# Kernel tuning notes

Measured on AMD Instinct MI355X. Metric: run time of the kernel, lower is better.

## Reference

```python
import jax, jax.numpy as jnp
from jax import lax
import numpy as np

D_MODEL = 512
D_STATE = 16
D_CONV = 4
EXPAND = 2
D_INNER = EXPAND * D_MODEL
DT_RANK = (D_MODEL + 15) // 16  # ceil(d_model/16) = 32
B, L = 4, 1024


def setup_inputs() -> dict:
    key = jax.random.key(0)
    ks = jax.random.split(key, 12)
    s = 0.02
    inp = {
        "feature": jax.random.normal(ks[0], (B, L, D_MODEL), jnp.float32),
        "ln_w": jnp.ones((D_MODEL,), jnp.float32),
        "ln_b": jnp.zeros((D_MODEL,), jnp.float32),
        "in_proj_w": jax.random.normal(ks[1], (2 * D_INNER, D_MODEL), jnp.float32) * s,
        "conv_w": jax.random.normal(ks[2], (D_INNER, D_CONV), jnp.float32) * 0.1,
        "conv_b": jnp.zeros((D_INNER,), jnp.float32),
        "x_proj_w": jax.random.normal(ks[3], (DT_RANK + 2 * D_STATE, D_INNER), jnp.float32) * s,
        "dt_proj_w": jax.random.normal(ks[4], (D_INNER, DT_RANK), jnp.float32) * 0.1,
        "dt_proj_b": jax.random.normal(ks[5], (D_INNER,), jnp.float32) * 0.1 - 4.0,
        "A_log": jnp.log(jnp.broadcast_to(jnp.arange(1, D_STATE + 1, dtype=jnp.float32), (D_INNER, D_STATE))),
        "D": jnp.ones((D_INNER,), jnp.float32),
        "out_proj_w": jax.random.normal(ks[6], (D_MODEL, D_INNER), jnp.float32) * s,
    }
    return inp


def _mamba_block(xn, in_proj_w, conv_w, conv_b, x_proj_w, dt_proj_w, dt_proj_b, A_log, D, out_proj_w):
    # xn: [B, L, d_model]
    xz = jnp.einsum('bld,ed->ble', xn, in_proj_w)          # [B, L, 2*d_inner]
    x, z = xz[..., :D_INNER], xz[..., D_INNER:]
    # causal depthwise conv along L
    xc = jnp.transpose(x, (0, 2, 1))                        # [B, d_inner, L]
    xc = lax.conv_general_dilated(
        xc, conv_w[:, None, :], (1,), [(D_CONV - 1, 0)],
        feature_group_count=D_INNER,
        dimension_numbers=('NCH', 'OIH', 'NCH')) + conv_b[None, :, None]
    x = jax.nn.silu(jnp.transpose(xc, (0, 2, 1)))           # [B, L, d_inner]
    x_dbl = jnp.einsum('bld,ed->ble', x, x_proj_w)          # [B, L, dt_rank+2*d_state]
    dt = x_dbl[..., :DT_RANK]
    Bm = x_dbl[..., DT_RANK:DT_RANK + D_STATE]
    Cm = x_dbl[..., DT_RANK + D_STATE:]
    dt = jax.nn.softplus(jnp.einsum('blr,dr->bld', dt, dt_proj_w) + dt_proj_b)  # [B,L,d_inner]
    A = -jnp.exp(A_log)                                     # [d_inner, d_state]

    def step(h, inp):
        dt_t, B_t, C_t, x_t = inp                           # [B,d_inner],[B,d_state],[B,d_state],[B,d_inner]
        dA = jnp.exp(dt_t[..., None] * A)                   # [B, d_inner, d_state]
        h = dA * h + (dt_t * x_t)[..., None] * B_t[:, None, :]
        y = jnp.einsum('bds,bs->bd', h, C_t)
        return h, y

    xs = (jnp.transpose(dt, (1, 0, 2)), jnp.transpose(Bm, (1, 0, 2)),
          jnp.transpose(Cm, (1, 0, 2)), jnp.transpose(x, (1, 0, 2)))
    h0 = jnp.zeros((xn.shape[0], D_INNER, D_STATE), xn.dtype)
    _, ys = lax.scan(step, h0, xs)                          # ys: [L, B, d_inner]
    y = jnp.transpose(ys, (1, 0, 2)) + x * D
    y = y * jax.nn.silu(z)
    return jnp.einsum('bld,ed->ble', y, out_proj_w)         # [B, L, d_model]


def reference(feature, ln_w, ln_b, in_proj_w, conv_w, conv_b, x_proj_w,
              dt_proj_w, dt_proj_b, A_log, D, out_proj_w):
    eps = 1e-5
    mu = jnp.mean(feature, axis=-1, keepdims=True)
    var = jnp.var(feature, axis=-1, keepdims=True)
    xn = (feature - mu) / jnp.sqrt(var + eps) * ln_w + ln_b
    out = _mamba_block(xn, in_proj_w, conv_w, conv_b, x_proj_w,
                       dt_proj_w, dt_proj_b, A_log, D, out_proj_w)
    return xn + out
```

## Files before the change

### kernel.cpp

```cpp
#include <hip/hip_runtime.h>
#include <hip/hip_bf16.h>
#include <math.h>

#define B_SZ 4
#define L_SZ 1024
#define DM   512
#define DI   1024
#define DS   16
#define DTR  32
#define NXD  64
#define M_ROWS (B_SZ*L_SZ)
#define CHK  32
#define CLEN 32
#define NCH  (B_SZ*DI)
#define PLANE (NCH*DS)
#define LDA  40

typedef __attribute__((ext_vector_type(8))) short short8;
typedef __attribute__((ext_vector_type(4))) float f32x4;
typedef __hip_bfloat16 bf16;

__device__ __forceinline__ float bf2f(bf16 x){ return __bfloat162float(x); }
__device__ __forceinline__ float fsig(float x){ return __builtin_amdgcn_rcpf(1.f + __expf(-x)); }
__device__ __forceinline__ unsigned short bfbits(float x){ bf16 b = __float2bfloat16(x); return *(unsigned short*)&b; }
#define LOG2E 1.44269504f

__device__ __forceinline__ bool is_f32(const void* lnw){
    return *(const unsigned*)lnw == 0x3F800000u;
}
__device__ __forceinline__ float loadf(const void* s, int i, bool f){
    return f ? ((const float*)s)[i] : bf2f(((const bf16*)s)[i]);
}
__device__ __forceinline__ bf16 loadb(const void* s, int i, bool f){
    return f ? __float2bfloat16(((const float*)s)[i]) : ((const bf16*)s)[i];
}

#define CVT_TOTAL 1694720
__global__ __launch_bounds__(256) void prep_kernel(
        const void* __restrict__ feat, const void* __restrict__ lnw, const void* __restrict__ lnb,
        const void* __restrict__ w_in, const void* __restrict__ w_x, const void* __restrict__ w_out,
        const void* __restrict__ w_dt, const void* __restrict__ b_dt,
        const void* __restrict__ alog, const void* __restrict__ dvec,
        const void* __restrict__ cw, const void* __restrict__ cb,
        bf16* __restrict__ WINB, bf16* __restrict__ WXB, bf16* __restrict__ WOUTB,
        float* __restrict__ WDTT, float* __restrict__ BDT, float* __restrict__ ALOG,
        float* __restrict__ DVEC, float* __restrict__ CWF, float* __restrict__ CBF,
        bf16* __restrict__ xnb, float* __restrict__ XDBL) {
    bool f = is_f32(lnw);
    if (blockIdx.y == 0) {
        int id = blockIdx.x*256 + threadIdx.x;
        if (id < M_ROWS*NXD) XDBL[id] = 0.f;
        #pragma unroll 2
        for (int g = id; g < CVT_TOTAL; g += 1048576) {
            if      (g < 1048576)  WINB[g] = loadb(w_in, g, f);
            else if (g < 1114112)  WXB[g-1048576] = loadb(w_x, g-1048576, f);
            else if (g < 1638400)  WOUTB[g-1114112] = loadb(w_out, g-1114112, f);
            else if (g < 1671168){ int i = g-1638400; WDTT[(i&(DTR-1))*DI + (i>>5)] = loadf(w_dt, i, f); }
            else if (g < 1672192)  BDT[g-1671168] = loadf(b_dt, g-1671168, f);
            else if (g < 1688576)  ALOG[g-1672192] = loadf(alog, g-1672192, f);
            else if (g < 1689600)  DVEC[g-1688576] = loadf(dvec, g-1688576, f);
            else if (g < 1693696)  CWF[g-1689600] = loadf(cw, g-1689600, f);
            else                   CBF[g-1693696] = loadf(cb, g-1693696, f);
        }
    } else {
        int row = blockIdx.x;
        int t = threadIdx.x;
        size_t base = (size_t)row*DM;
        float v0 = loadf(feat, base+t, f);
        float v1 = loadf(feat, base+t+256, f);
        __shared__ float ssum[256], ssq[256];
        ssum[t] = v0+v1; ssq[t] = v0*v0+v1*v1;
        __syncthreads();
        for (int off=128; off>0; off>>=1){
            if (t<off){ ssum[t]+=ssum[t+off]; ssq[t]+=ssq[t+off]; }
            __syncthreads();
        }
        float mu  = ssum[0]*(1.0f/DM);
        float var = ssq[0]*(1.0f/DM) - mu*mu;
        float rstd = rsqrtf(var + 1e-5f);
        float o0 = (v0-mu)*rstd*loadf(lnw,t,f)     + loadf(lnb,t,f);
        float o1 = (v1-mu)*rstd*loadf(lnw,t+256,f) + loadf(lnb,t+256,f);
        xnb[base + t]     = __float2bfloat16(o0);
        xnb[base + t+256] = __float2bfloat16(o1);
    }
}


__global__ __launch_bounds__(256) void gemm_in_mfma(const bf16* __restrict__ A,
        const bf16* __restrict__ W, bf16* __restrict__ XB, bf16* __restrict__ ZB) {
    const int K = 512;
    __shared__ bf16 As[128*LDA];
    __shared__ bf16 Bs[128*LDA];
    int t = threadIdx.x;
    int w = t>>6, l = t&63;
    int wm = w&1, wn = w>>1;
    int row0 = blockIdx.y*128, col0 = blockIdx.x*128;
    int lr = l&15, lq = l>>4;
    int srow = t>>2, scol = (t&3)*8;
    const bf16* pA0 = A + (size_t)(row0+srow)*K    + scol;
    const bf16* pA1 = A + (size_t)(row0+64+srow)*K + scol;
    const bf16* pB0 = W + (size_t)(col0+srow)*K    + scol;
    const bf16* pB1 = W + (size_t)(col0+64+srow)*K + scol;
    f32x4 acc[4][4] = {};
    short8 a0 = *(const short8*)(pA0);
    short8 a1 = *(const short8*)(pA1);
    short8 b0 = *(const short8*)(pB0);
    short8 b1 = *(const short8*)(pB1);
    for (int k0=0; k0<K; k0+=32) {
        __syncthreads();
        *(short8*)(As + srow*LDA + scol)      = a0;
        *(short8*)(As + (64+srow)*LDA + scol) = a1;
        *(short8*)(Bs + srow*LDA + scol)      = b0;
        *(short8*)(Bs + (64+srow)*LDA + scol) = b1;
        __syncthreads();
        if (k0 + 32 < K) {
            a0 = *(const short8*)(pA0 + k0 + 32);
            a1 = *(const short8*)(pA1 + k0 + 32);
            b0 = *(const short8*)(pB0 + k0 + 32);
            b1 = *(const short8*)(pB1 + k0 + 32);
        }
        short8 af[4], bfr[4];
        #pragma unroll
        for (int mi=0;mi<4;mi++) af[mi]  = *(const short8*)(As + (wm*64+mi*16+lr)*LDA + lq*8);
        #pragma unroll
        for (int ni=0;ni<4;ni++) bfr[ni] = *(const short8*)(Bs + (wn*64+ni*16+lr)*LDA + lq*8);
        #pragma unroll
        for (int mi=0;mi<4;mi++)
            #pragma unroll
            for (int ni=0;ni<4;ni++)
                acc[mi][ni] = __builtin_amdgcn_mfma_f32_16x16x32_bf16(af[mi], bfr[ni], acc[mi][ni], 0,0,0);
    }
    bf16* dst; int cbn;
    if (col0 < DI) { dst = XB; cbn = col0; } else { dst = ZB; cbn = col0 - DI; }
    #pragma unroll
    for (int mi=0;mi<4;mi++)
        #pragma unroll
        for (int ni=0;ni<4;ni++) {
            int r = row0 + wm*64 + mi*16 + lq*4;
            int c = cbn  + wn*64 + ni*16 + lr;
            #pragma unroll
            for (int rr=0;rr<4;rr++)
                dst[(size_t)(r+rr)*DI + c] = __float2bfloat16(acc[mi][ni][rr]);
        }
}

__global__ __launch_bounds__(256) void gemm_xc_mfma(const bf16* __restrict__ XB,
        const bf16* __restrict__ W, const float* __restrict__ cw, const float* __restrict__ cb,
        bf16* __restrict__ XC, float* __restrict__ C) {
    const int K = 1024;
    __shared__ bf16 As[64*LDA];
    __shared__ bf16 Bs[64*LDA];
    int t = threadIdx.x;
    int w = t>>6, l64 = t&63;
    int wm = w&1, wn = w>>1;
    int row0 = blockIdx.y*64;
    int kbeg = blockIdx.x*(K/4), kend = kbeg + K/4;
    int lr = l64&15, lq = l64>>4;
    int srow = t>>2, scol = (t&3)*8;
    int m = row0 + srow;
    int lpos = m & (L_SZ-1);
    bool vr0 = lpos >= 3, vr1 = lpos >= 2, vr2 = lpos >= 1;
    const bf16* pxb = XB + (size_t)(m-3)*DI + kbeg + scol;
    const bf16* pB0 = W + (size_t)srow*K + kbeg + scol;
    f32x4 acc[2][2] = {};
    short8 x0 = *(const short8*)(pxb);
    short8 x1 = *(const short8*)(pxb + DI);
    short8 x2 = *(const short8*)(pxb + 2*DI);
    short8 x3 = *(const short8*)(pxb + 3*DI);
    short8 b0 = *(const short8*)(pB0);
    for (int k0=kbeg; k0<kend; k0+=32) {
        int dbase = k0 + scol;
        short8 xx0 = x0, xx1 = x1, xx2 = x2;
        if (!vr0) xx0 = (short8){0,0,0,0,0,0,0,0};
        if (!vr1) xx1 = (short8){0,0,0,0,0,0,0,0};
        if (!vr2) xx2 = (short8){0,0,0,0,0,0,0,0};
        uint a0[4], a1[4], a2[4], a3[4];
        *(uint4*)a0 = *(uint4*)&xx0; *(uint4*)a1 = *(uint4*)&xx1;
        *(uint4*)a2 = *(uint4*)&xx2; *(uint4*)a3 = *(uint4*)&x3;
        uint outw[4];
        #pragma unroll
        for (int jw=0; jw<4; jw++){
            float r2[2];
            #pragma unroll
            for (int hi=0; hi<2; hi++){
                int dch = dbase + jw*2 + hi;
                float4 wv = *(const float4*)(cw + (size_t)dch*4);
                float accv = cb[dch];
                float e0 = hi ? __uint_as_float(a0[jw] & 0xffff0000u) : __uint_as_float(a0[jw] << 16);
                float e1 = hi ? __uint_as_float(a1[jw] & 0xffff0000u) : __uint_as_float(a1[jw] << 16);
                float e2 = hi ? __uint_as_float(a2[jw] & 0xffff0000u) : __uint_as_float(a2[jw] << 16);
                float e3 = hi ? __uint_as_float(a3[jw] & 0xffff0000u) : __uint_as_float(a3[jw] << 16);
                accv = fmaf(e0, wv.x, accv); accv = fmaf(e1, wv.y, accv);
                accv = fmaf(e2, wv.z, accv); accv = fmaf(e3, wv.w, accv);
                r2[hi] = accv * fsig(accv);
            }
            outw[jw] = (uint)bfbits(r2[0]) | ((uint)bfbits(r2[1]) << 16);
        }
        short8 cv; *(uint4*)&cv = *(uint4*)outw;
        __syncthreads();
        *(short8*)(As + srow*LDA + scol) = cv;
        *(short8*)(Bs + srow*LDA + scol) = b0;
        __syncthreads();
        *(short8*)(XC + (size_t)m*DI + dbase) = cv;
        if (k0 + 32 < kend) {
            pxb += 32; pB0 += 32;
            x0 = *(const short8*)(pxb);
            x1 = *(const short8*)(pxb + DI);
            x2 = *(const short8*)(pxb + 2*DI);
            x3 = *(const short8*)(pxb + 3*DI);
            b0 = *(const short8*)(pB0);
        }
        short8 af[2], bfr[2];
        #pragma unroll
        for (int mi=0;mi<2;mi++) af[mi]  = *(const short8*)(As + (wm*32+mi*16+lr)*LDA + lq*8);
        #pragma unroll
        for (int ni=0;ni<2;ni++) bfr[ni] = *(const short8*)(Bs + (wn*32+ni*16+lr)*LDA + lq*8);
        #pragma unroll
        for (int mi=0;mi<2;mi++)
            #pragma unroll
            for (int ni=0;ni<2;ni++)
                acc[mi][ni] = __builtin_amdgcn_mfma_f32_16x16x32_bf16(af[mi], bfr[ni], acc[mi][ni], 0,0,0);
    }
    #pragma unroll
    for (int mi=0;mi<2;mi++)
        #pragma unroll
        for (int ni=0;ni<2;ni++) {
            int r = row0 + wm*32 + mi*16 + lq*4;
            int c = wn*32 + ni*16 + lr;
            #pragma unroll
            for (int rr=0;rr<4;rr++)
                atomicAdd(&C[(size_t)(r+rr)*NXD + c], acc[mi][ni][rr]);
        }
}

__global__ __launch_bounds__(256) void gemm_out_mfma(const bf16* __restrict__ A,
        const bf16* __restrict__ W, const bf16* __restrict__ xnb,
        void* __restrict__ out, const void* __restrict__ lnw) {
    const int K = 1024;
    __shared__ bf16 As[128*LDA];
    __shared__ bf16 Bs[128*LDA];
    int t = threadIdx.x;
    int w = t>>6, l = t&63;
    int wm = w&1, wn = w>>1;
    int row0 = blockIdx.y*128, col0 = blockIdx.x*128;
    int lr = l&15, lq = l>>4;
    int srow = t>>2, scol = (t&3)*8;
    const bf16* pA0 = A + (size_t)(row0+srow)*K    + scol;
    const bf16* pA1 = A + (size_t)(row0+64+srow)*K + scol;
    const bf16* pB0 = W + (size_t)(col0+srow)*K    + scol;
    const bf16* pB1 = W + (size_t)(col0+64+srow)*K + scol;
    f32x4 acc[4][4] = {};
    short8 a0 = *(const short8*)(pA0);
    short8 a1 = *(const short8*)(pA1);
    short8 b0 = *(const short8*)(pB0);
    short8 b1 = *(const short8*)(pB1);
    for (int k0=0; k0<K; k0+=32) {
        __syncthreads();
        *(short8*)(As + srow*LDA + scol)      = a0;
        *(short8*)(As + (64+srow)*LDA + scol) = a1;
        *(short8*)(Bs + srow*LDA + scol)      = b0;
        *(short8*)(Bs + (64+srow)*LDA + scol) = b1;
        __syncthreads();
        if (k0 + 32 < K) {
            a0 = *(const short8*)(pA0 + k0 + 32);
            a1 = *(const short8*)(pA1 + k0 + 32);
            b0 = *(const short8*)(pB0 + k0 + 32);
            b1 = *(const short8*)(pB1 + k0 + 32);
        }
        short8 af[4], bfr[4];
        #pragma unroll
        for (int mi=0;mi<4;mi++) af[mi]  = *(const short8*)(As + (wm*64+mi*16+lr)*LDA + lq*8);
        #pragma unroll
        for (int ni=0;ni<4;ni++) bfr[ni] = *(const short8*)(Bs + (wn*64+ni*16+lr)*LDA + lq*8);
        #pragma unroll
        for (int mi=0;mi<4;mi++)
            #pragma unroll
            for (int ni=0;ni<4;ni++)
                acc[mi][ni] = __builtin_amdgcn_mfma_f32_16x16x32_bf16(af[mi], bfr[ni], acc[mi][ni], 0,0,0);
    }
    bool f = is_f32(lnw);
    #pragma unroll
    for (int mi=0;mi<4;mi++)
        #pragma unroll
        for (int ni=0;ni<4;ni++) {
            int r = row0 + wm*64 + mi*16 + lq*4;
            int c = col0 + wn*64 + ni*16 + lr;
            #pragma unroll
            for (int rr=0;rr<4;rr++) {
                float v = acc[mi][ni][rr] + bf2f(xnb[(size_t)(r+rr)*DM + c]);
                if (f) ((float*)out)[(size_t)(r+rr)*DM + c] = v;
                else   ((bf16*)out)[(size_t)(r+rr)*DM + c] = __float2bfloat16(v);
            }
        }
}


__global__ __launch_bounds__(256) void scan_p1(const bf16* __restrict__ xc,
        const float* __restrict__ xdbl, const float* __restrict__ dtwT,
        const float* __restrict__ dtb, const float* __restrict__ A_log,
        float* __restrict__ SP, float* __restrict__ PP) {
    int ch = blockIdx.x*256 + threadIdx.x;
    int j  = blockIdx.y;
    int d  = ch & (DI-1);
    int bu = __builtin_amdgcn_readfirstlane(ch >> 10);
    float a2[DS];
    {
        const float4* pa = (const float4*)(A_log + d*DS);
        #pragma unroll
        for (int q=0;q<4;q++){
            float4 v = pa[q];
            a2[q*4+0] = -__expf(v.x)*LOG2E; a2[q*4+1] = -__expf(v.y)*LOG2E;
            a2[q*4+2] = -__expf(v.z)*LOG2E; a2[q*4+3] = -__expf(v.w)*LOG2E;
        }
    }
    float wdt[DTR];
    #pragma unroll
    for (int r=0;r<DTR;r++) wdt[r] = dtwT[r*DI + d];
    float bias = dtb[d];
    float h[DS], P[DS];
    #pragma unroll
    for (int s=0;s<DS;s++){ h[s]=0.f; P[s]=1.f; }
    size_t row = (size_t)bu*L_SZ + (size_t)j*CLEN;
    const bf16* pxc = xc  + row*DI + d;
    const float* pX = xdbl + row*NXD;
    #pragma unroll 2
    for (int t=0; t<CLEN; t++) {
        float acc = bias;
        #pragma unroll
        for (int r=0;r<DTR;r++) acc = fmaf(pX[r], wdt[r], acc);
        float dt = (acc > 20.f) ? acc : __logf(1.f + __expf(acc));
        float u  = dt * bf2f(*pxc);
        const float* pB = pX + DTR;
        #pragma unroll
        for (int s=0;s<DS;s++){
            float dA = __builtin_exp2f(dt*a2[s]);
            h[s] = fmaf(dA, h[s], u*pB[s]);
            P[s] *= dA;
        }
        pxc += DI; pX += NXD;
    }
    float* sp = SP + (size_t)j*PLANE + ch;
    float* pp = PP + (size_t)j*PLANE + ch;
    #pragma unroll
    for (int s=0;s<DS;s++){ sp[s*NCH] = h[s]; pp[s*NCH] = P[s]; }
}

__global__ void scan_p2(const float* __restrict__ SP, const float* __restrict__ PP,
                        float* __restrict__ HB) {
    int idx = blockIdx.x*256 + threadIdx.x;
    float H = 0.f;
    for (int j=0;j<CHK;j++){
        size_t o = (size_t)j*PLANE + idx;
        float p = PP[o], s = SP[o];
        HB[o] = H;
        H = fmaf(p, H, s);
    }
}

__global__ __launch_bounds__(256) void scan_p3(const bf16* __restrict__ xc,
        const float* __restrict__ xdbl, const float* __restrict__ dtwT,
        const float* __restrict__ dtb, const float* __restrict__ A_log,
        const float* __restrict__ Dp, const float* __restrict__ HB,
        const bf16* __restrict__ zb, bf16* __restrict__ ybf) {
    int ch = blockIdx.x*256 + threadIdx.x;
    int j  = blockIdx.y;
    int d  = ch & (DI-1);
    int bu = __builtin_amdgcn_readfirstlane(ch >> 10);
    float a2[DS];
    {
        const float4* pa = (const float4*)(A_log + d*DS);
        #pragma unroll
        for (int q=0;q<4;q++){
            float4 v = pa[q];
            a2[q*4+0] = -__expf(v.x)*LOG2E; a2[q*4+1] = -__expf(v.y)*LOG2E;
            a2[q*4+2] = -__expf(v.z)*LOG2E; a2[q*4+3] = -__expf(v.w)*LOG2E;
        }
    }
    float wdt[DTR];
    #pragma unroll
    for (int r=0;r<DTR;r++) wdt[r] = dtwT[r*DI + d];
    float bias = dtb[d];
    float h[DS];
    {
        const float* ph = HB + (size_t)j*PLANE + ch;
        #pragma unroll
        for (int s=0;s<DS;s++) h[s] = ph[s*NCH];
    }
    float Dd = Dp[d];
    size_t row = (size_t)bu*L_SZ + (size_t)j*CLEN;
    const bf16* pxc = xc  + row*DI + d;
    const float* pX = xdbl + row*NXD;
    const bf16* pz  = zb  + row*DI + d;
    bf16*       py  = ybf + row*DI + d;
    #pragma unroll 2
    for (int t=0; t<CLEN; t++) {
        float acc = bias;
        #pragma unroll
        for (int r=0;r<DTR;r++) acc = fmaf(pX[r], wdt[r], acc);
        float dt = (acc > 20.f) ? acc : __logf(1.f + __expf(acc));
        float xv = bf2f(*pxc);
        float u  = dt * xv;
        const float* pB = pX + DTR;
        const float* pC = pX + DTR + DS;
        float y0=0.f, y1=0.f, y2=0.f, y3=0.f;
        #pragma unroll
        for (int s=0;s<DS;s+=4){
            float dA0 = __builtin_exp2f(dt*a2[s]);
            float dA1 = __builtin_exp2f(dt*a2[s+1]);
            float dA2 = __builtin_exp2f(dt*a2[s+2]);
            float dA3 = __builtin_exp2f(dt*a2[s+3]);
            h[s]   = fmaf(dA0, h[s],   u*pB[s]);
            h[s+1] = fmaf(dA1, h[s+1], u*pB[s+1]);
            h[s+2] = fmaf(dA2, h[s+2], u*pB[s+2]);
            h[s+3] = fmaf(dA3, h[s+3], u*pB[s+3]);
            y0 = fmaf(h[s],   pC[s],   y0);
            y1 = fmaf(h[s+1], pC[s+1], y1);
            y2 = fmaf(h[s+2], pC[s+2], y2);
            y3 = fmaf(h[s+3], pC[s+3], y3);
        }
        float y = (y0+y1) + (y2+y3) + xv*Dd;
        float z = bf2f(*pz);
        *py = __float2bfloat16(y * z * fsig(z));
        pxc += DI; pX += NXD; pz += DI; py += DI;
    }
}

extern "C" void kernel_launch(void* const* d_in, const int* in_sizes, int n_in,
                              void* d_out, int out_size, void* d_ws, size_t ws_size,
                              hipStream_t stream) {
    float* FW = (float*)d_ws;
    float* SP   = FW;
    float* PP   = FW + 2097152;
    float* HB   = FW + 4194304;
    bf16*  XNB  = (bf16*)(FW + 6291456);
    float* XDBL = FW + 7340032;
    float* WDTT = FW + 7602176;
    float* BDT  = FW + 7634944;
    float* ALOG = FW + 7635968;
    float* DVEC = FW + 7652352;
    float* CWF  = FW + 7653376;
    float* CBF  = FW + 7657472;
    bf16* XBB  = (bf16*)(FW + 7658496);
    bf16* YBF  = XBB;
    bf16* ZBB  = (bf16*)(FW + 9755648);
    bf16* XCB  = (bf16*)(FW + 11852800);
    bf16* WINB = (bf16*)(FW + 13949952);
    bf16* WXB  = (bf16*)(FW + 14474240);
    bf16* WOUTB= (bf16*)(FW + 14507008);

    prep_kernel<<<dim3(4096, 2), 256, 0, stream>>>(
        d_in[0], d_in[1], d_in[2], d_in[3], d_in[6], d_in[11], d_in[7], d_in[8],
        d_in[9], d_in[10], d_in[4], d_in[5],
        WINB, WXB, WOUTB, WDTT, BDT, ALOG, DVEC, CWF, CBF, XNB, XDBL);
    gemm_in_mfma<<<dim3(2048/128, M_ROWS/128), 256, 0, stream>>>(XNB, WINB, XBB, ZBB);
    gemm_xc_mfma<<<dim3(4, M_ROWS/64), 256, 0, stream>>>(XBB, WXB, CWF, CBF, XCB, XDBL);
    scan_p1<<<dim3(NCH/256, CHK), 256, 0, stream>>>(XCB, XDBL, WDTT, BDT, ALOG, SP, PP);
    scan_p2<<<PLANE/256, 256, 0, stream>>>(SP, PP, HB);
    scan_p3<<<dim3(NCH/256, CHK), 256, 0, stream>>>(XCB, XDBL, WDTT, BDT, ALOG, DVEC, HB, ZBB, YBF);
    gemm_out_mfma<<<dim3(DM/128, M_ROWS/128), 256, 0, stream>>>(YBF, WOUTB, XNB, d_out, d_in[1]);
}
```

Baseline: 224.7 us.

## Shorten scan chunks, widen xc K-split, narrow out GEMM tiles, bf16 scan states

The chunked scan now uses 64 chunks of length 16 instead of 32 chunks of 32, which gives the scan kernels more parallel blocks and shorter sequential loops. The x_proj GEMM splits K eight ways instead of four, adding more blocks but also more atomic adds. The output GEMM moves from 128x128 to 128x64 tiles, doubling the block count. The chunk carry states (SP, PP, HB) are stored in bf16 rather than fp32 to cut memory traffic, at the cost of lower precision in the inter-chunk recurrence.

Result: faster. 209.6 us (-6.7%).

```diff
diff --git a/kernel.cpp b/kernel.cpp
--- a/kernel.cpp
+++ b/kernel.cpp
@@ -10,11 +10,12 @@
 #define DTR  32
 #define NXD  64
 #define M_ROWS (B_SZ*L_SZ)
-#define CHK  32
-#define CLEN 32
+#define CHK  64
+#define CLEN 16
 #define NCH  (B_SZ*DI)
 #define PLANE (NCH*DS)
 #define LDA  40
+#define KSPL 8
 
 typedef __attribute__((ext_vector_type(8))) short short8;
 typedef __attribute__((ext_vector_type(4))) float f32x4;
@@ -154,7 +155,7 @@
     int w = t>>6, l64 = t&63;
     int wm = w&1, wn = w>>1;
     int row0 = blockIdx.y*64;
-    int kbeg = blockIdx.x*(K/4), kend = kbeg + K/4;
+    int kbeg = blockIdx.x*(K/KSPL), kend = kbeg + K/KSPL;
     int lr = l64&15, lq = l64>>4;
     int srow = t>>2, scol = (t&3)*8;
     int m = row0 + srow;
@@ -238,53 +239,49 @@
         void* __restrict__ out, const void* __restrict__ lnw) {
     const int K = 1024;
     __shared__ bf16 As[128*LDA];
-    __shared__ bf16 Bs[128*LDA];
+    __shared__ bf16 Bs[64*LDA];
     int t = threadIdx.x;
     int w = t>>6, l = t&63;
     int wm = w&1, wn = w>>1;
-    int row0 = blockIdx.y*128, col0 = blockIdx.x*128;
+    int row0 = blockIdx.y*128, col0 = blockIdx.x*64;
     int lr = l&15, lq = l>>4;
     int srow = t>>2, scol = (t&3)*8;
     const bf16* pA0 = A + (size_t)(row0+srow)*K    + scol;
     const bf16* pA1 = A + (size_t)(row0+64+srow)*K + scol;
     const bf16* pB0 = W + (size_t)(col0+srow)*K    + scol;
-    const bf16* pB1 = W + (size_t)(col0+64+srow)*K + scol;
-    f32x4 acc[4][4] = {};
+    f32x4 acc[4][2] = {};
     short8 a0 = *(const short8*)(pA0);
     short8 a1 = *(const short8*)(pA1);
     short8 b0 = *(const short8*)(pB0);
-    short8 b1 = *(const short8*)(pB1);
     for (int k0=0; k0<K; k0+=32) {
         __syncthreads();
         *(short8*)(As + srow*LDA + scol)      = a0;
         *(short8*)(As + (64+srow)*LDA + scol) = a1;
         *(short8*)(Bs + srow*LDA + scol)      = b0;
-        *(short8*)(Bs + (64+srow)*LDA + scol) = b1;
         __syncthreads();
         if (k0 + 32 < K) {
             a0 = *(const short8*)(pA0 + k0 + 32);
             a1 = *(const short8*)(pA1 + k0 + 32);
             b0 = *(const short8*)(pB0 + k0 + 32);
-            b1 = *(const short8*)(pB1 + k0 + 32);
-        }
-        short8 af[4], bfr[4];
+        }
+        short8 af[4], bfr[2];
         #pragma unroll
         for (int mi=0;mi<4;mi++) af[mi]  = *(const short8*)(As + (wm*64+mi*16+lr)*LDA + lq*8);
         #pragma unroll
-        for (int ni=0;ni<4;ni++) bfr[ni] = *(const short8*)(Bs + (wn*64+ni*16+lr)*LDA + lq*8);
+        for (int ni=0;ni<2;ni++) bfr[ni] = *(const short8*)(Bs + (wn*32+ni*16+lr)*LDA + lq*8);
         #pragma unroll
         for (int mi=0;mi<4;mi++)
             #pragma unroll
-            for (int ni=0;ni<4;ni++)
+            for (int ni=0;ni<2;ni++)
                 acc[mi][ni] = __builtin_amdgcn_mfma_f32_16x16x32_bf16(af[mi], bfr[ni], acc[mi][ni], 0,0,0);
     }
     bool f = is_f32(lnw);
     #pragma unroll
     for (int mi=0;mi<4;mi++)
         #pragma unroll
-        for (int ni=0;ni<4;ni++) {
+        for (int ni=0;ni<2;ni++) {
             int r = row0 + wm*64 + mi*16 + lq*4;
-            int c = col0 + wn*64 + ni*16 + lr;
+            int c = col0 + wn*32 + ni*16 + lr;
             #pragma unroll
             for (int rr=0;rr<4;rr++) {
                 float v = acc[mi][ni][rr] + bf2f(xnb[(size_t)(r+rr)*DM + c]);
@@ -298,7 +295,7 @@
 __global__ __launch_bounds__(256) void scan_p1(const bf16* __restrict__ xc,
         const float* __restrict__ xdbl, const float* __restrict__ dtwT,
         const float* __restrict__ dtb, const float* __restrict__ A_log,
-        float* __restrict__ SP, float* __restrict__ PP) {
+        bf16* __restrict__ SP, bf16* __restrict__ PP) {
     int ch = blockIdx.x*256 + threadIdx.x;
     int j  = blockIdx.y;
     int d  = ch & (DI-1);
@@ -339,20 +336,20 @@
         }
         pxc += DI; pX += NXD;
     }
-    float* sp = SP + (size_t)j*PLANE + ch;
-    float* pp = PP + (size_t)j*PLANE + ch;
-    #pragma unroll
-    for (int s=0;s<DS;s++){ sp[s*NCH] = h[s]; pp[s*NCH] = P[s]; }
-}
-
-__global__ void scan_p2(const float* __restrict__ SP, const float* __restrict__ PP,
-                        float* __restrict__ HB) {
+    bf16* sp = SP + (size_t)j*PLANE + ch;
+    bf16* pp = PP + (size_t)j*PLANE + ch;
+    #pragma unroll
+    for (int s=0;s<DS;s++){ sp[s*NCH] = __float2bfloat16(h[s]); pp[s*NCH] = __float2bfloat16(P[s]); }
+}
+
+__global__ void scan_p2(const bf16* __restrict__ SP, const bf16* __restrict__ PP,
+                        bf16* __restrict__ HB) {
     int idx = blockIdx.x*256 + threadIdx.x;
     float H = 0.f;
     for (int j=0;j<CHK;j++){
         size_t o = (size_t)j*PLANE + idx;
-        float p = PP[o], s = SP[o];
-        HB[o] = H;
+        float p = bf2f(PP[o]), s = bf2f(SP[o]);
+        HB[o] = __float2bfloat16(H);
         H = fmaf(p, H, s);
     }
 }
@@ -360,7 +357,7 @@
 __global__ __launch_bounds__(256) void scan_p3(const bf16* __restrict__ xc,
         const float* __restrict__ xdbl, const float* __restrict__ dtwT,
         const float* __restrict__ dtb, const float* __restrict__ A_log,
-        const float* __restrict__ Dp, const float* __restrict__ HB,
+        const float* __restrict__ Dp, const bf16* __restrict__ HB,
         const bf16* __restrict__ zb, bf16* __restrict__ ybf) {
     int ch = blockIdx.x*256 + threadIdx.x;
     int j  = blockIdx.y;
@@ -382,9 +379,9 @@
     float bias = dtb[d];
     float h[DS];
     {
-        const float* ph = HB + (size_t)j*PLANE + ch;
-        #pragma unroll
-        for (int s=0;s<DS;s++) h[s] = ph[s*NCH];
+        const bf16* ph = HB + (size_t)j*PLANE + ch;
+        #pragma unroll
+        for (int s=0;s<DS;s++) h[s] = bf2f(ph[s*NCH]);
     }
     float Dd = Dp[d];
     size_t row = (size_t)bu*L_SZ + (size_t)j*CLEN;
@@ -429,9 +426,9 @@
                               void* d_out, int out_size, void* d_ws, size_t ws_size,
                               hipStream_t stream) {
     float* FW = (float*)d_ws;
-    float* SP   = FW;
-    float* PP   = FW + 2097152;
-    float* HB   = FW + 4194304;
+    bf16*  SPB  = (bf16*)FW;
+    bf16*  PPB  = (bf16*)(FW + 2097152);
+    bf16*  HBB  = (bf16*)(FW + 4194304);
     bf16*  XNB  = (bf16*)(FW + 6291456);
     float* XDBL = FW + 7340032;
     float* WDTT = FW + 7602176;
@@ -453,9 +450,9 @@
         d_in[9], d_in[10], d_in[4], d_in[5],
         WINB, WXB, WOUTB, WDTT, BDT, ALOG, DVEC, CWF, CBF, XNB, XDBL);
     gemm_in_mfma<<<dim3(2048/128, M_ROWS/128), 256, 0, stream>>>(XNB, WINB, XBB, ZBB);
-    gemm_xc_mfma<<<dim3(4, M_ROWS/64), 256, 0, stream>>>(XBB, WXB, CWF, CBF, XCB, XDBL);
-    scan_p1<<<dim3(NCH/256, CHK), 256, 0, stream>>>(XCB, XDBL, WDTT, BDT, ALOG, SP, PP);
-    scan_p2<<<PLANE/256, 256, 0, stream>>>(SP, PP, HB);
-    scan_p3<<<dim3(NCH/256, CHK), 256, 0, stream>>>(XCB, XDBL, WDTT, BDT, ALOG, DVEC, HB, ZBB, YBF);
-    gemm_out_mfma<<<dim3(DM/128, M_ROWS/128), 256, 0, stream>>>(YBF, WOUTB, XNB, d_out, d_in[1]);
-}
+    gemm_xc_mfma<<<dim3(KSPL, M_ROWS/64), 256, 0, stream>>>(XBB, WXB, CWF, CBF, XCB, XDBL);
+    scan_p1<<<dim3(NCH/256, CHK), 256, 0, stream>>>(XCB, XDBL, WDTT, BDT, ALOG, SPB, PPB);
+    scan_p2<<<PLANE/256, 256, 0, stream>>>(SPB, PPB, HBB);
+    scan_p3<<<dim3(NCH/256, CHK), 256, 0, stream>>>(XCB, XDBL, WDTT, BDT, ALOG, DVEC, HBB, ZBB, YBF);
+    gemm_out_mfma<<<dim3(DM/64, M_ROWS/128), 256, 0, stream>>>(YBF, WOUTB, XNB, d_out, d_in[1]);
+}
```
